# Kernel optimization log

Hardware: AMD Instinct MI355X
Metric: run time of the kernel (lower is better)

Reference implementation:

```python
import jax, jax.numpy as jnp
import numpy as np

N_NODES = 100000
N_EDGES = 3200000
NFEAT = 128
NHID = 128
NCLASS = 8
BN_EPS = 1e-5


def setup_inputs() -> dict:
    key = jax.random.key(0)
    ks = jax.random.split(key, 8)
    x = jax.random.normal(ks[0], (N_NODES, NFEAT), dtype=jnp.float32)
    edge_index = jax.random.randint(ks[1], (2, N_EDGES), 0, N_NODES, dtype=jnp.int64)
    # GCNConv params: weight [nfeat, nhid] (glorot), bias [nhid]
    lim = float(np.sqrt(6.0 / (NFEAT + NHID)))
    W = jax.random.uniform(ks[2], (NFEAT, NHID), minval=-lim, maxval=lim, dtype=jnp.float32)
    b_gc = jnp.zeros((NHID,), dtype=jnp.float32)
    # BatchNorm1d params
    gamma = jnp.ones((NHID,), dtype=jnp.float32)
    beta = jnp.zeros((NHID,), dtype=jnp.float32)
    # fc head: (nhid/2) -> nclass, xavier_uniform, zero bias
    lim2 = float(np.sqrt(6.0 / (NHID // 2 + NCLASS)))
    fc_w = jax.random.uniform(ks[3], (NCLASS, NHID // 2), minval=-lim2, maxval=lim2, dtype=jnp.float32)
    fc_b = jnp.zeros((NCLASS,), dtype=jnp.float32)
    return {"x": x, "edge_index": edge_index, "W": W, "b_gc": b_gc,
            "gamma": gamma, "beta": beta, "fc_w": fc_w, "fc_b": fc_b}


def _gcn_conv(x, edge_index, W, b):
    """PyG GCNConv: add self-loops, symmetric norm, linear, gather-scatter, bias."""
    N = x.shape[0]
    loops = jnp.arange(N, dtype=edge_index.dtype)
    src = jnp.concatenate([edge_index[0], loops])  # source (row / x_j)
    dst = jnp.concatenate([edge_index[1], loops])  # target (col / aggregation index)
    # degree of target nodes (edge weight = 1)
    deg = jax.ops.segment_sum(jnp.ones_like(dst, dtype=x.dtype), dst, num_segments=N)
    dinv = jnp.where(deg > 0, jax.lax.rsqrt(deg), 0.0)
    norm = dinv[src] * dinv[dst]  # [E+N]
    h = x @ W  # [N, nhid]
    msg = h[src] * norm[:, None]  # gather + scale
    out = jax.ops.segment_sum(msg, dst, num_segments=N)  # scatter-add
    return out + b


def _batchnorm(h, gamma, beta):
    mean = jnp.mean(h, axis=0)
    var = jnp.mean(jnp.square(h - mean), axis=0)  # biased, training-mode
    return gamma * (h - mean) * jax.lax.rsqrt(var + BN_EPS) + beta


def reference(x, edge_index, W, b_gc, gamma, beta, fc_w, fc_b):
    h = _gcn_conv(x, edge_index, W, b_gc)
    embed = _batchnorm(h, gamma, beta)
    half = embed.shape[1] // 2
    out = embed[:, :half] @ fc_w.T + fc_b
    return (out, embed)
```

## Files before the change

### kernel.cpp

```cpp
#include <hip/hip_runtime.h>
#include <hip/hip_bf16.h>
#include <math.h>

#define N_NODES 100000
#define N_EDGES 3200000
#define NFEAT 128
#define NHID 128
#define NCLASS 8
#define BN_EPS 1e-5f
#define CB 512
#define NBC 196
#define EPB 8192
#define PART_BLOCKS 391
#define GEMM_BLOCKS 1563

typedef __attribute__((ext_vector_type(8))) short short8;
typedef __attribute__((ext_vector_type(4))) float f32x4;

__device__ __forceinline__ short f2bf(float f) {
    __hip_bfloat16 b = __float2bfloat16(f);
    return *reinterpret_cast<short*>(&b);
}
__device__ __forceinline__ float bf_lo(unsigned u) { return __uint_as_float(u << 16); }
__device__ __forceinline__ float bf_hi(unsigned u) { return __uint_as_float(u & 0xffff0000u); }


#define WSTRIDE 136
#define XSTRIDE 136
__global__ __launch_bounds__(256) void k_prep(const float* __restrict__ x,
                                              const float* __restrict__ W,
                                              unsigned short* __restrict__ hb,
                                              const int* __restrict__ dst,
                                              int* __restrict__ ghist) {
    __shared__ __align__(16) short wlds[NHID * WSTRIDE];
    __shared__ __align__(16) short xl[64 * XSTRIDE];
    const int tid = threadIdx.x;

    if (blockIdx.x >= GEMM_BLOCKS) {
        __shared__ int lh[NBC];
        if (tid < NBC) lh[tid] = 0;
        __syncthreads();
        const int4* dst4 = (const int4*)dst;
        const int q0 = (blockIdx.x - GEMM_BLOCKS) * (EPB / 4) + tid;
#pragma unroll
        for (int i = 0; i < 8; ++i) {
            int q = q0 + i * 256;
            if (q < N_EDGES / 4) {
                int4 d = dst4[q];
                atomicAdd(&lh[d.x >> 9], 1);
                atomicAdd(&lh[d.y >> 9], 1);
                atomicAdd(&lh[d.z >> 9], 1);
                atomicAdd(&lh[d.w >> 9], 1);
            }
        }
        __syncthreads();
        if (tid < NBC) {
            int c = lh[tid];
            if (c) atomicAdd(&ghist[tid], c);
        }
        return;
    }

    const int row0 = blockIdx.x * 64;

#pragma unroll 8
    for (int i = 0; i < 64; ++i) {
        int idx = tid + i * 256;
        int k = idx >> 7, n = idx & 127;
        wlds[n * WSTRIDE + k] = f2bf(W[idx]);
    }
    const float4* x4 = (const float4*)x;
#pragma unroll
    for (int i = 0; i < 8; ++i) {
        int idx = tid + i * 256;
        int r = idx >> 5, c4 = idx & 31;
        int gr = row0 + r;
        float4 vv = (gr < N_NODES) ? x4[(size_t)gr * 32 + c4]
                                   : (float4){0.f, 0.f, 0.f, 0.f};
        short4 t;
        t.x = f2bf(vv.x); t.y = f2bf(vv.y); t.z = f2bf(vv.z); t.w = f2bf(vv.w);
        *(short4*)&xl[r * XSTRIDE + c4 * 4] = t;
    }
    __syncthreads();

    const int wid = tid >> 6, lane = tid & 63;
    const int qw = lane >> 4, lr = lane & 15;

    short8 a[4];
#pragma unroll
    for (int ks = 0; ks < 4; ++ks)
        a[ks] = *(const short8*)&xl[(wid * 16 + lr) * XSTRIDE + ks * 32 + qw * 8];

    f32x4 acc[8];
#pragma unroll
    for (int nt = 0; nt < 8; ++nt) acc[nt] = (f32x4){0.f, 0.f, 0.f, 0.f};

#pragma unroll
    for (int nt = 0; nt < 8; ++nt) {
#pragma unroll
        for (int ks = 0; ks < 4; ++ks) {
            short8 bfr = *(const short8*)&wlds[(nt * 16 + lr) * WSTRIDE + ks * 32 + qw * 8];
            acc[nt] = __builtin_amdgcn_mfma_f32_16x16x32_bf16(a[ks], bfr, acc[nt], 0, 0, 0);
        }
    }

    const int rbase = row0 + wid * 16 + qw * 4;
#pragma unroll
    for (int j = 0; j < 4; ++j) {
        int r = rbase + j;
        if (r >= N_NODES) continue;
#pragma unroll
        for (int nt = 0; nt < 8; ++nt)
            hb[(size_t)r * NHID + nt * 16 + lr] = (unsigned short)f2bf(acc[nt][j]);
    }
}


__global__ __launch_bounds__(512) void k_cscan(const int* __restrict__ ghist,
                                               int* __restrict__ coff,
                                               int* __restrict__ ccur,
                                               int* __restrict__ off,
                                               float* __restrict__ stats,
                                               int* __restrict__ ticket,
                                               unsigned short* __restrict__ hbzrow,
                                               float* __restrict__ dinv) {
    __shared__ int tmp[512];
    const int t = threadIdx.x;
    if (t < 256) stats[t] = 0.f;
    if (t == 0) { *ticket = 0; dinv[N_NODES] = 0.f; }
    if (t < NHID) hbzrow[t] = 0;
    int v = (t < NBC) ? ghist[t] : 0;
    tmp[t] = v;
    __syncthreads();
    for (int d = 1; d < 512; d <<= 1) {
        int u = (t >= d) ? tmp[t - d] : 0;
        __syncthreads();
        tmp[t] += u;
        __syncthreads();
    }
    int excl = tmp[t] - v;
    if (t < NBC) {
        coff[t] = excl;
        ccur[t] = excl;
    }
    if (t == NBC - 1) {
        coff[NBC] = tmp[t];
        off[N_NODES] = tmp[t];
    }
}


__global__ __launch_bounds__(256) void k_part(const int* __restrict__ src,
                                              const int* __restrict__ dst,
                                              int* __restrict__ ccur,
                                              unsigned* __restrict__ epack) {
    __shared__ int lh[NBC];
    __shared__ int lstart[NBC];
    __shared__ int adj[NBC];
    __shared__ int stmp[256];
    __shared__ unsigned sorted[EPB];
    __shared__ unsigned char bkt[EPB];
    const int tid = threadIdx.x;
    if (tid < NBC) lh[tid] = 0;
    __syncthreads();
    const int4* src4 = (const int4*)src;
    const int4* dst4 = (const int4*)dst;
    const int q0 = blockIdx.x * (EPB / 4) + tid;
    int4 sv[8], dv[8];
    int rk[32];
#pragma unroll
    for (int i = 0; i < 8; ++i) {
        int q = q0 + i * 256;
        if (q < N_EDGES / 4) {
            sv[i] = src4[q];
            dv[i] = dst4[q];
            rk[i * 4 + 0] = atomicAdd(&lh[dv[i].x >> 9], 1);
            rk[i * 4 + 1] = atomicAdd(&lh[dv[i].y >> 9], 1);
            rk[i * 4 + 2] = atomicAdd(&lh[dv[i].z >> 9], 1);
            rk[i * 4 + 3] = atomicAdd(&lh[dv[i].w >> 9], 1);
        } else dv[i].x = -1;
    }
    __syncthreads();
    int v = (tid < NBC) ? lh[tid] : 0;
    stmp[tid] = v;
    __syncthreads();
    for (int d = 1; d < 256; d <<= 1) {
        int u = (tid >= d) ? stmp[tid - d] : 0;
        __syncthreads();
        stmp[tid] += u;
        __syncthreads();
    }
    if (tid < NBC) {
        int ls = stmp[tid] - v;
        lstart[tid] = ls;
        adj[tid] = (v ? atomicAdd(&ccur[tid], v) : 0) - ls;
    }
    __syncthreads();
#pragma unroll
    for (int i = 0; i < 8; ++i) {
        if (dv[i].x >= 0) {
            int b, p;
            b = dv[i].x >> 9; p = lstart[b] + rk[i * 4 + 0];
            sorted[p] = ((unsigned)sv[i].x << 9) | (unsigned)(dv[i].x & 511); bkt[p] = (unsigned char)b;
            b = dv[i].y >> 9; p = lstart[b] + rk[i * 4 + 1];
            sorted[p] = ((unsigned)sv[i].y << 9) | (unsigned)(dv[i].y & 511); bkt[p] = (unsigned char)b;
            b = dv[i].z >> 9; p = lstart[b] + rk[i * 4 + 2];
            sorted[p] = ((unsigned)sv[i].z << 9) | (unsigned)(dv[i].z & 511); bkt[p] = (unsigned char)b;
            b = dv[i].w >> 9; p = lstart[b] + rk[i * 4 + 3];
            sorted[p] = ((unsigned)sv[i].w << 9) | (unsigned)(dv[i].w & 511); bkt[p] = (unsigned char)b;
        }
    }
    __syncthreads();
    const int vcnt = stmp[255];
    for (int p = tid; p < vcnt; p += 256)
        epack[p + adj[bkt[p]]] = sorted[p];
}


__global__ __launch_bounds__(256) void k_fine(const unsigned* __restrict__ epack,
                                              const int* __restrict__ coff,
                                              int* __restrict__ off,
                                              float* __restrict__ dinv,
                                              int* __restrict__ esrc) {
    __shared__ int lh[CB], lcur[CB], lsc[256];
    const int tid = threadIdx.x;
    const int b = blockIdx.x;
    const int node0 = b << 9;
    lh[tid] = 0;
    lh[tid + 256] = 0;
    __syncthreads();
    const int lo = coff[b], hiEnd = coff[b + 1];
    for (int i = lo + tid; i < hiEnd; i += 256)
        atomicAdd(&lh[epack[i] & 511u], 1);
    __syncthreads();
    int v0 = lh[2 * tid], v1 = lh[2 * tid + 1];
    int s = v0 + v1;
    lsc[tid] = s;
    __syncthreads();
    for (int d = 1; d < 256; d <<= 1) {
        int u = (tid >= d) ? lsc[tid - d] : 0;
        __syncthreads();
        lsc[tid] += u;
        __syncthreads();
    }
    int pairExcl = lsc[tid] - s;
    lcur[2 * tid] = pairExcl;
    lcur[2 * tid + 1] = pairExcl + v0;
    int n0 = node0 + 2 * tid, n1 = n0 + 1;
    if (n0 < N_NODES) { off[n0] = lo + pairExcl;      dinv[n0] = rsqrtf((float)(v0 + 1)); }
    if (n1 < N_NODES) { off[n1] = lo + pairExcl + v0; dinv[n1] = rsqrtf((float)(v1 + 1)); }
    __syncthreads();
    for (int i = lo + tid; i < hiEnd; i += 256) {
        unsigned p = epack[i];
        int pos = atomicAdd(&lcur[p & 511u], 1);
        esrc[lo + pos] = (int)(p >> 9);
    }
}


__global__ __launch_bounds__(256) void k_agg(const int* __restrict__ off,
                                             const int* __restrict__ esrc,
                                             const float* __restrict__ dinv,
                                             const uint2* __restrict__ hbq,
                                             float4* __restrict__ agg4) {
    const int node = (blockIdx.x << 2) | (threadIdx.x >> 6);
    const int lane = threadIdx.x & 63;
    const int hl = lane >> 5;
    const int cl = lane & 31;
    if (node >= N_NODES) return;

    const float dn = dinv[node];
    const int self = hl ? N_NODES : node;
    uint2 u0 = hbq[(size_t)self * 32 + cl];
    float aAx = dn * bf_lo(u0.x), aAy = dn * bf_hi(u0.x);
    float aAz = dn * bf_lo(u0.y), aAw = dn * bf_hi(u0.y);
    float aBx = 0.f, aBy = 0.f, aBz = 0.f, aBw = 0.f;
    float aCx = 0.f, aCy = 0.f, aCz = 0.f, aCw = 0.f;
    float aDx = 0.f, aDy = 0.f, aDz = 0.f, aDw = 0.f;

    const int begin = off[node], end = off[node + 1];
    for (int base = begin; base < end; base += 64) {
        int m = end - base;
        if (m > 64) m = 64;
        int sv = N_NODES;
        float dw = 0.f;
        if (lane < m) {
            sv = esrc[base + lane];
            dw = dinv[sv];
        }
        const int kmax = (m + 7) >> 3;
        for (int k = 0; k < kmax; ++k) {
            int sA = __shfl(sv, 8 * k + 0 + hl);
            int sB = __shfl(sv, 8 * k + 2 + hl);
            int sC = __shfl(sv, 8 * k + 4 + hl);
            int sD = __shfl(sv, 8 * k + 6 + hl);
            float wA = __shfl(dw, 8 * k + 0 + hl);
            float wB = __shfl(dw, 8 * k + 2 + hl);
            float wC = __shfl(dw, 8 * k + 4 + hl);
            float wD = __shfl(dw, 8 * k + 6 + hl);
            uint2 uA = hbq[(size_t)sA * 32 + cl];
            uint2 uB = hbq[(size_t)sB * 32 + cl];
            uint2 uC = hbq[(size_t)sC * 32 + cl];
            uint2 uD = hbq[(size_t)sD * 32 + cl];
            aAx = fmaf(wA, bf_lo(uA.x), aAx); aAy = fmaf(wA, bf_hi(uA.x), aAy);
            aAz = fmaf(wA, bf_lo(uA.y), aAz); aAw = fmaf(wA, bf_hi(uA.y), aAw);
            aBx = fmaf(wB, bf_lo(uB.x), aBx); aBy = fmaf(wB, bf_hi(uB.x), aBy);
            aBz = fmaf(wB, bf_lo(uB.y), aBz); aBw = fmaf(wB, bf_hi(uB.y), aBw);
            aCx = fmaf(wC, bf_lo(uC.x), aCx); aCy = fmaf(wC, bf_hi(uC.x), aCy);
            aCz = fmaf(wC, bf_lo(uC.y), aCz); aCw = fmaf(wC, bf_hi(uC.y), aCw);
            aDx = fmaf(wD, bf_lo(uD.x), aDx); aDy = fmaf(wD, bf_hi(uD.x), aDy);
            aDz = fmaf(wD, bf_lo(uD.y), aDz); aDw = fmaf(wD, bf_hi(uD.y), aDw);
        }
    }
    float ax = (aAx + aBx) + (aCx + aDx);
    float ay = (aAy + aBy) + (aCy + aDy);
    float az = (aAz + aBz) + (aCz + aDz);
    float aw = (aAw + aBw) + (aCw + aDw);
    ax += __shfl_xor(ax, 32);
    ay += __shfl_xor(ay, 32);
    az += __shfl_xor(az, 32);
    aw += __shfl_xor(aw, 32);
    if (hl == 0) {
        float4 o;
        o.x = ax * dn; o.y = ay * dn; o.z = az * dn; o.w = aw * dn;
        agg4[(size_t)node * 32 + cl] = o;
    }
}


__global__ __launch_bounds__(256) void k_stats(const float* __restrict__ agg,
                                               float* __restrict__ stats,
                                               int* __restrict__ ticket,
                                               const float* __restrict__ gamma,
                                               const float* __restrict__ beta,
                                               float* __restrict__ ss) {
    const int cb = threadIdx.x & 31;
    const int rg = threadIdx.x >> 5;
    const float4* a4 = (const float4*)agg;
    float4 s = {0.f, 0.f, 0.f, 0.f}, s2 = {0.f, 0.f, 0.f, 0.f};
    for (int r = blockIdx.x * 8 + rg; r < N_NODES; r += gridDim.x * 8) {
        float4 v = a4[(size_t)r * 32 + cb];
        s.x += v.x; s.y += v.y; s.z += v.z; s.w += v.w;
        s2.x += v.x * v.x; s2.y += v.y * v.y; s2.z += v.z * v.z; s2.w += v.w * v.w;
    }
    __shared__ float4 ls[256], ls2[256];
    __shared__ int lastflag;
    ls[threadIdx.x] = s;
    ls2[threadIdx.x] = s2;
    __syncthreads();
    if (rg == 0) {
        float4 ts = ls[cb], t2 = ls2[cb];
#pragma unroll
        for (int g = 1; g < 8; ++g) {
            float4 v = ls[g * 32 + cb], w = ls2[g * 32 + cb];
            ts.x += v.x; ts.y += v.y; ts.z += v.z; ts.w += v.w;
            t2.x += w.x; t2.y += w.y; t2.z += w.z; t2.w += w.w;
        }
        atomicAdd(&stats[cb * 4 + 0], ts.x);
        atomicAdd(&stats[cb * 4 + 1], ts.y);
        atomicAdd(&stats[cb * 4 + 2], ts.z);
        atomicAdd(&stats[cb * 4 + 3], ts.w);
        atomicAdd(&stats[128 + cb * 4 + 0], t2.x);
        atomicAdd(&stats[128 + cb * 4 + 1], t2.y);
        atomicAdd(&stats[128 + cb * 4 + 2], t2.z);
        atomicAdd(&stats[128 + cb * 4 + 3], t2.w);
    }
    __threadfence();
    __syncthreads();
    if (threadIdx.x == 0)
        lastflag = (atomicAdd(ticket, 1) == (int)gridDim.x - 1) ? 1 : 0;
    __syncthreads();
    if (lastflag && threadIdx.x < NHID) {
        int c = threadIdx.x;
        float sum = atomicAdd(&stats[c], 0.f);
        float sq  = atomicAdd(&stats[128 + c], 0.f);
        float mean = sum / (float)N_NODES;
        float var = fmaxf(sq / (float)N_NODES - mean * mean, 0.f);
        float inv = rsqrtf(var + BN_EPS);
        float sc = gamma[c] * inv;
        ss[c] = sc;
        ss[128 + c] = beta[c] - mean * sc;
    }
}


__global__ __launch_bounds__(256) void k_bnfc(float* __restrict__ embed,
                                              const float* __restrict__ ss,
                                              const float* __restrict__ fc_w,
                                              const float* __restrict__ fc_b,
                                              float* __restrict__ out) {
    __shared__ float se[64][68];
    __shared__ float sw[8][68];
    __shared__ float sb[8];
    const int tid = threadIdx.x;
    const int row0 = blockIdx.x * 64;
    {
        int d = tid;
        sw[d >> 6][d & 63] = fc_w[d];
        d = tid + 256;
        sw[d >> 6][d & 63] = fc_w[d];
        if (tid < 8) sb[tid] = fc_b[tid];
    }
    float4* ef4 = (float4*)embed;
    const float4* ssc4 = (const float4*)ss;
    const float4* ssh4 = (const float4*)(ss + 128);
#pragma unroll
    for (int i = 0; i < 8; ++i) {
        int d = tid + i * 256;
        int r = d >> 5;
        int cb = d & 31;
        int gr = row0 + r;
        if (gr < N_NODES) {
            float4 v = ef4[(size_t)gr * 32 + cb];
            float4 sc = ssc4[cb], sh = ssh4[cb];
            v.x = fmaf(v.x, sc.x, sh.x);
            v.y = fmaf(v.y, sc.y, sh.y);
            v.z = fmaf(v.z, sc.z, sh.z);
            v.w = fmaf(v.w, sc.w, sh.w);
            ef4[(size_t)gr * 32 + cb] = v;
            if (cb < 16) {
                se[r][cb * 4 + 0] = v.x; se[r][cb * 4 + 1] = v.y;
                se[r][cb * 4 + 2] = v.z; se[r][cb * 4 + 3] = v.w;
            }
        } else if (cb < 16) {
            se[r][cb * 4 + 0] = 0.f; se[r][cb * 4 + 1] = 0.f;
            se[r][cb * 4 + 2] = 0.f; se[r][cb * 4 + 3] = 0.f;
        }
    }
    __syncthreads();
    const int r = tid >> 2;
    const int j0 = (tid & 3) * 2;
    const int gr = row0 + r;
#pragma unroll
    for (int jj = 0; jj < 2; ++jj) {
        int j = j0 + jj;
        float s = sb[j];
#pragma unroll
        for (int k = 0; k < 64; ++k) s = fmaf(se[r][k], sw[j][k], s);
        if (gr < N_NODES) out[(size_t)gr * NCLASS + j] = s;
    }
}


extern "C" void kernel_launch(void* const* d_in, const int* in_sizes, int n_in,
                              void* d_out, int out_size, void* d_ws, size_t ws_size,
                              hipStream_t stream) {
    const float* x     = (const float*)d_in[0];
    const int*   ei    = (const int*)d_in[1];
    const float* W     = (const float*)d_in[2];
    const float* gamma = (const float*)d_in[4];
    const float* beta  = (const float*)d_in[5];
    const float* fc_w  = (const float*)d_in[6];
    const float* fc_b  = (const float*)d_in[7];

    const int* src = ei;
    const int* dst = ei + N_EDGES;

    float* out   = (float*)d_out;
    float* embed = (float*)d_out + (size_t)N_NODES * NCLASS;

    char* ws = (char*)d_ws;
    size_t o = 0;
    unsigned* epack = (unsigned*)(ws + o);          o += (size_t)N_EDGES * 4;
    unsigned short* hb = (unsigned short*)(ws + o); o += (size_t)(N_NODES + 1) * NHID * 2;
    o = (o + 255) & ~(size_t)255;
    int* esrc   = (int*)(ws + o);                   o += (size_t)N_EDGES * 4;
    int* off    = (int*)(ws + o);                   o += (size_t)(N_NODES + 1) * 4;
    float* dinv = (float*)(ws + o);                 o += (size_t)(N_NODES + 1) * 4;
    float* stats = (float*)(ws + o);                o += 256 * 4;
    float* ss    = (float*)(ws + o);                o += 256 * 4;
    int* ghist   = (int*)(ws + o);                  o += NBC * 4;
    int* coff    = (int*)(ws + o);                  o += (NBC + 1) * 4;
    int* ccur    = (int*)(ws + o);                  o += NBC * 4;
    int* ticket  = (int*)(ws + o);                  o += 4;

    hipMemsetAsync(ghist, 0, NBC * 4, stream);

    k_prep<<<GEMM_BLOCKS + PART_BLOCKS, 256, 0, stream>>>(x, W, hb, dst, ghist);

    k_cscan<<<1, 512, 0, stream>>>(ghist, coff, ccur, off, stats, ticket,
                                   hb + (size_t)N_NODES * NHID, dinv);
    k_part<<<PART_BLOCKS, 256, 0, stream>>>(src, dst, ccur, epack);
    k_fine<<<NBC, 256, 0, stream>>>(epack, coff, off, dinv, esrc);

    k_agg<<<(N_NODES + 3) / 4, 256, 0, stream>>>(off, esrc, dinv, (const uint2*)hb, (float4*)embed);

    k_stats<<<512, 256, 0, stream>>>(embed, stats, ticket, gamma, beta, ss);

    k_bnfc<<<(N_NODES + 63) / 64, 256, 0, stream>>>(embed, ss, fc_w, fc_b, out);
}
```

Baseline: 320.7 us.

## Prescale GEMM output by source dinv and fuse partition into GEMM launch

Per-node in-degrees are now counted with global atomics in a new count kernel, so dinv is ready before the GEMM. The GEMM epilogue multiplies each row by dinv[src], which lets the aggregation loop drop the per-edge dinv gather and its shuffles and use plain adds. The edge-partition pass is merged into the same launch as the GEMM so the two overlap. In exchange the count kernel adds 3.2M global atomics on per-node counters, and k_gp needs a larger shared-memory footprint.

```diff
diff --git a/kernel.cpp b/kernel.cpp
--- a/kernel.cpp
+++ b/kernel.cpp
@@ -25,49 +25,161 @@
 __device__ __forceinline__ float bf_hi(unsigned u) { return __uint_as_float(u & 0xffff0000u); }
 
 
-#define WSTRIDE 136
-#define XSTRIDE 136
-__global__ __launch_bounds__(256) void k_prep(const float* __restrict__ x,
-                                              const float* __restrict__ W,
-                                              unsigned short* __restrict__ hb,
-                                              const int* __restrict__ dst,
-                                              int* __restrict__ ghist) {
-    __shared__ __align__(16) short wlds[NHID * WSTRIDE];
-    __shared__ __align__(16) short xl[64 * XSTRIDE];
+__global__ __launch_bounds__(256) void k_cnt(const int* __restrict__ dst,
+                                             int* __restrict__ cnt,
+                                             int* __restrict__ ghist) {
+    __shared__ int lh[NBC];
     const int tid = threadIdx.x;
+    if (tid < NBC) lh[tid] = 0;
+    __syncthreads();
+    const int4* dst4 = (const int4*)dst;
+    const int q0 = blockIdx.x * (EPB / 4) + tid;
+#pragma unroll
+    for (int i = 0; i < 8; ++i) {
+        int q = q0 + i * 256;
+        if (q < N_EDGES / 4) {
+            int4 d = dst4[q];
+            atomicAdd(&cnt[d.x], 1);
+            atomicAdd(&cnt[d.y], 1);
+            atomicAdd(&cnt[d.z], 1);
+            atomicAdd(&cnt[d.w], 1);
+            atomicAdd(&lh[d.x >> 9], 1);
+            atomicAdd(&lh[d.y >> 9], 1);
+            atomicAdd(&lh[d.z >> 9], 1);
+            atomicAdd(&lh[d.w >> 9], 1);
+        }
+    }
+    __syncthreads();
+    if (tid < NBC) {
+        int c = lh[tid];
+        if (c) atomicAdd(&ghist[tid], c);
+    }
+}
+
+
+__global__ __launch_bounds__(512) void k_scan(const int* __restrict__ ghist,
+                                              const int* __restrict__ cnt,
+                                              int* __restrict__ coff,
+                                              int* __restrict__ ccur,
+                                              int* __restrict__ off,
+                                              float* __restrict__ dinv,
+                                              float* __restrict__ stats,
+                                              int* __restrict__ ticket,
+                                              unsigned short* __restrict__ hbzrow) {
+    const int t = threadIdx.x;
+    if (blockIdx.x > 0) {
+        int node = (blockIdx.x - 1) * 512 + t;
+        if (node < N_NODES) dinv[node] = rsqrtf((float)(cnt[node] + 1));
+        return;
+    }
+    __shared__ int tmp[512];
+    if (t < 256) stats[t] = 0.f;
+    if (t == 0) *ticket = 0;
+    if (t < NHID) hbzrow[t] = 0;
+    int v = (t < NBC) ? ghist[t] : 0;
+    tmp[t] = v;
+    __syncthreads();
+    for (int d = 1; d < 512; d <<= 1) {
+        int u = (t >= d) ? tmp[t - d] : 0;
+        __syncthreads();
+        tmp[t] += u;
+        __syncthreads();
+    }
+    int excl = tmp[t] - v;
+    if (t < NBC) {
+        coff[t] = excl;
+        ccur[t] = excl;
+    }
+    if (t == NBC - 1) {
+        coff[NBC] = tmp[t];
+        off[N_NODES] = tmp[t];
+    }
+}
+
+
+__global__ __launch_bounds__(256) void k_gp(const float* __restrict__ x,
+                                            const float* __restrict__ W,
+                                            const float* __restrict__ dinv,
+                                            unsigned short* __restrict__ hb,
+                                            const int* __restrict__ src,
+                                            const int* __restrict__ dst,
+                                            int* __restrict__ ccur,
+                                            unsigned* __restrict__ epack) {
+    __shared__ __align__(16) char smem[52224];
+    const int tid = threadIdx.x;
 
     if (blockIdx.x >= GEMM_BLOCKS) {
-        __shared__ int lh[NBC];
+        unsigned* sorted = (unsigned*)smem;
+        unsigned char* bkt = (unsigned char*)(smem + 32768);
+        int* lh     = (int*)(smem + 40960);
+        int* lstart = (int*)(smem + 40960 + 784);
+        int* adj    = (int*)(smem + 40960 + 1568);
+        int* stmp   = (int*)(smem + 40960 + 2352);
         if (tid < NBC) lh[tid] = 0;
         __syncthreads();
+        const int4* src4 = (const int4*)src;
         const int4* dst4 = (const int4*)dst;
         const int q0 = (blockIdx.x - GEMM_BLOCKS) * (EPB / 4) + tid;
+        int4 sv[8], dv[8];
+        int rk[32];
 #pragma unroll
         for (int i = 0; i < 8; ++i) {
             int q = q0 + i * 256;
             if (q < N_EDGES / 4) {
-                int4 d = dst4[q];
-                atomicAdd(&lh[d.x >> 9], 1);
-                atomicAdd(&lh[d.y >> 9], 1);
-                atomicAdd(&lh[d.z >> 9], 1);
-                atomicAdd(&lh[d.w >> 9], 1);
+                sv[i] = src4[q];
+                dv[i] = dst4[q];
+                rk[i * 4 + 0] = atomicAdd(&lh[dv[i].x >> 9], 1);
+                rk[i * 4 + 1] = atomicAdd(&lh[dv[i].y >> 9], 1);
+                rk[i * 4 + 2] = atomicAdd(&lh[dv[i].z >> 9], 1);
+                rk[i * 4 + 3] = atomicAdd(&lh[dv[i].w >> 9], 1);
+            } else dv[i].x = -1;
+        }
+        __syncthreads();
+        int v = (tid < NBC) ? lh[tid] : 0;
+        stmp[tid] = v;
+        __syncthreads();
+        for (int d = 1; d < 256; d <<= 1) {
+            int u = (tid >= d) ? stmp[tid - d] : 0;
+            __syncthreads();
+            stmp[tid] += u;
+            __syncthreads();
+        }
+        if (tid < NBC) {
+            int ls = stmp[tid] - v;
+            lstart[tid] = ls;
+            adj[tid] = (v ? atomicAdd(&ccur[tid], v) : 0) - ls;
+        }
+        __syncthreads();
+#pragma unroll
+        for (int i = 0; i < 8; ++i) {
+            if (dv[i].x >= 0) {
+                int b, p;
+                b = dv[i].x >> 9; p = lstart[b] + rk[i * 4 + 0];
+                sorted[p] = ((unsigned)sv[i].x << 9) | (unsigned)(dv[i].x & 511); bkt[p] = (unsigned char)b;
+                b = dv[i].y >> 9; p = lstart[b] + rk[i * 4 + 1];
+                sorted[p] = ((unsigned)sv[i].y << 9) | (unsigned)(dv[i].y & 511); bkt[p] = (unsigned char)b;
+                b = dv[i].z >> 9; p = lstart[b] + rk[i * 4 + 2];
+                sorted[p] = ((unsigned)sv[i].z << 9) | (unsigned)(dv[i].z & 511); bkt[p] = (unsigned char)b;
+                b = dv[i].w >> 9; p = lstart[b] + rk[i * 4 + 3];
+                sorted[p] = ((unsigned)sv[i].w << 9) | (unsigned)(dv[i].w & 511); bkt[p] = (unsigned char)b;
             }
         }
         __syncthreads();
-        if (tid < NBC) {
-            int c = lh[tid];
-            if (c) atomicAdd(&ghist[tid], c);
-        }
+        const int vcnt = stmp[255];
+        for (int p = tid; p < vcnt; p += 256)
+            epack[p + adj[bkt[p]]] = sorted[p];
         return;
     }
 
+    short* wlds = (short*)smem;
+    short* xl   = (short*)(smem + 34816);
     const int row0 = blockIdx.x * 64;
 
 #pragma unroll 8
     for (int i = 0; i < 64; ++i) {
         int idx = tid + i * 256;
         int k = idx >> 7, n = idx & 127;
-        wlds[n * WSTRIDE + k] = f2bf(W[idx]);
+        wlds[n * 136 + k] = f2bf(W[idx]);
     }
     const float4* x4 = (const float4*)x;
 #pragma unroll
@@ -79,7 +191,7 @@
                                    : (float4){0.f, 0.f, 0.f, 0.f};
         short4 t;
         t.x = f2bf(vv.x); t.y = f2bf(vv.y); t.z = f2bf(vv.z); t.w = f2bf(vv.w);
-        *(short4*)&xl[r * XSTRIDE + c4 * 4] = t;
+        *(short4*)&xl[r * 136 + c4 * 4] = t;
     }
     __syncthreads();
 
@@ -89,7 +201,7 @@
     short8 a[4];
 #pragma unroll
     for (int ks = 0; ks < 4; ++ks)
-        a[ks] = *(const short8*)&xl[(wid * 16 + lr) * XSTRIDE + ks * 32 + qw * 8];
+        a[ks] = *(const short8*)&xl[(wid * 16 + lr) * 136 + ks * 32 + qw * 8];
 
     f32x4 acc[8];
 #pragma unroll
@@ -99,128 +211,29 @@
     for (int nt = 0; nt < 8; ++nt) {
 #pragma unroll
         for (int ks = 0; ks < 4; ++ks) {
-            short8 bfr = *(const short8*)&wlds[(nt * 16 + lr) * WSTRIDE + ks * 32 + qw * 8];
+            short8 bfr = *(const short8*)&wlds[(nt * 16 + lr) * 136 + ks * 32 + qw * 8];
             acc[nt] = __builtin_amdgcn_mfma_f32_16x16x32_bf16(a[ks], bfr, acc[nt], 0, 0, 0);
         }
     }
 
     const int rbase = row0 + wid * 16 + qw * 4;
+    float dvv[4];
+#pragma unroll
+    for (int j = 0; j < 4; ++j) dvv[j] = (rbase + j < N_NODES) ? dinv[rbase + j] : 0.f;
 #pragma unroll
     for (int j = 0; j < 4; ++j) {
         int r = rbase + j;
         if (r >= N_NODES) continue;
 #pragma unroll
         for (int nt = 0; nt < 8; ++nt)
-            hb[(size_t)r * NHID + nt * 16 + lr] = (unsigned short)f2bf(acc[nt][j]);
-    }
-}
-
-
-__global__ __launch_bounds__(512) void k_cscan(const int* __restrict__ ghist,
-                                               int* __restrict__ coff,
-                                               int* __restrict__ ccur,
-                                               int* __restrict__ off,
-                                               float* __restrict__ stats,
-                                               int* __restrict__ ticket,
-                                               unsigned short* __restrict__ hbzrow,
-                                               float* __restrict__ dinv) {
-    __shared__ int tmp[512];
-    const int t = threadIdx.x;
-    if (t < 256) stats[t] = 0.f;
-    if (t == 0) { *ticket = 0; dinv[N_NODES] = 0.f; }
-    if (t < NHID) hbzrow[t] = 0;
-    int v = (t < NBC) ? ghist[t] : 0;
-    tmp[t] = v;
-    __syncthreads();
-    for (int d = 1; d < 512; d <<= 1) {
-        int u = (t >= d) ? tmp[t - d] : 0;
-        __syncthreads();
-        tmp[t] += u;
-        __syncthreads();
-    }
-    int excl = tmp[t] - v;
-    if (t < NBC) {
-        coff[t] = excl;
-        ccur[t] = excl;
-    }
-    if (t == NBC - 1) {
-        coff[NBC] = tmp[t];
-        off[N_NODES] = tmp[t];
-    }
-}
-
-
-__global__ __launch_bounds__(256) void k_part(const int* __restrict__ src,
-                                              const int* __restrict__ dst,
-                                              int* __restrict__ ccur,
-                                              unsigned* __restrict__ epack) {
-    __shared__ int lh[NBC];
-    __shared__ int lstart[NBC];
-    __shared__ int adj[NBC];
-    __shared__ int stmp[256];
-    __shared__ unsigned sorted[EPB];
-    __shared__ unsigned char bkt[EPB];
-    const int tid = threadIdx.x;
-    if (tid < NBC) lh[tid] = 0;
-    __syncthreads();
-    const int4* src4 = (const int4*)src;
-    const int4* dst4 = (const int4*)dst;
-    const int q0 = blockIdx.x * (EPB / 4) + tid;
-    int4 sv[8], dv[8];
-    int rk[32];
-#pragma unroll
-    for (int i = 0; i < 8; ++i) {
-        int q = q0 + i * 256;
-        if (q < N_EDGES / 4) {
-            sv[i] = src4[q];
-            dv[i] = dst4[q];
-            rk[i * 4 + 0] = atomicAdd(&lh[dv[i].x >> 9], 1);
-            rk[i * 4 + 1] = atomicAdd(&lh[dv[i].y >> 9], 1);
-            rk[i * 4 + 2] = atomicAdd(&lh[dv[i].z >> 9], 1);
-            rk[i * 4 + 3] = atomicAdd(&lh[dv[i].w >> 9], 1);
-        } else dv[i].x = -1;
-    }
-    __syncthreads();
-    int v = (tid < NBC) ? lh[tid] : 0;
-    stmp[tid] = v;
-    __syncthreads();
-    for (int d = 1; d < 256; d <<= 1) {
-        int u = (tid >= d) ? stmp[tid - d] : 0;
-        __syncthreads();
-        stmp[tid] += u;
-        __syncthreads();
-    }
-    if (tid < NBC) {
-        int ls = stmp[tid] - v;
-        lstart[tid] = ls;
-        adj[tid] = (v ? atomicAdd(&ccur[tid], v) : 0) - ls;
-    }
-    __syncthreads();
-#pragma unroll
-    for (int i = 0; i < 8; ++i) {
-        if (dv[i].x >= 0) {
-            int b, p;
-            b = dv[i].x >> 9; p = lstart[b] + rk[i * 4 + 0];
-            sorted[p] = ((unsigned)sv[i].x << 9) | (unsigned)(dv[i].x & 511); bkt[p] = (unsigned char)b;
-            b = dv[i].y >> 9; p = lstart[b] + rk[i * 4 + 1];
-            sorted[p] = ((unsigned)sv[i].y << 9) | (unsigned)(dv[i].y & 511); bkt[p] = (unsigned char)b;
-            b = dv[i].z >> 9; p = lstart[b] + rk[i * 4 + 2];
-            sorted[p] = ((unsigned)sv[i].z << 9) | (unsigned)(dv[i].z & 511); bkt[p] = (unsigned char)b;
-            b = dv[i].w >> 9; p = lstart[b] + rk[i * 4 + 3];
-            sorted[p] = ((unsigned)sv[i].w << 9) | (unsigned)(dv[i].w & 511); bkt[p] = (unsigned char)b;
-        }
-    }
-    __syncthreads();
-    const int vcnt = stmp[255];
-    for (int p = tid; p < vcnt; p += 256)
-        epack[p + adj[bkt[p]]] = sorted[p];
+            hb[(size_t)r * NHID + nt * 16 + lr] = (unsigned short)f2bf(dvv[j] * acc[nt][j]);
+    }
 }
 
 
 __global__ __launch_bounds__(256) void k_fine(const unsigned* __restrict__ epack,
                                               const int* __restrict__ coff,
                                               int* __restrict__ off,
-                                              float* __restrict__ dinv,
                                               int* __restrict__ esrc) {
     __shared__ int lh[CB], lcur[CB], lsc[256];
     const int tid = threadIdx.x;
@@ -247,8 +260,8 @@
     lcur[2 * tid] = pairExcl;
     lcur[2 * tid + 1] = pairExcl + v0;
     int n0 = node0 + 2 * tid, n1 = n0 + 1;
-    if (n0 < N_NODES) { off[n0] = lo + pairExcl;      dinv[n0] = rsqrtf((float)(v0 + 1)); }
-    if (n1 < N_NODES) { off[n1] = lo + pairExcl + v0; dinv[n1] = rsqrtf((float)(v1 + 1)); }
+    if (n0 < N_NODES) off[n0] = lo + pairExcl;
+    if (n1 < N_NODES) off[n1] = lo + pairExcl + v0;
     __syncthreads();
     for (int i = lo + tid; i < hiEnd; i += 256) {
         unsigned p = epack[i];
@@ -272,8 +285,7 @@
     const float dn = dinv[node];
     const int self = hl ? N_NODES : node;
     uint2 u0 = hbq[(size_t)self * 32 + cl];
-    float aAx = dn * bf_lo(u0.x), aAy = dn * bf_hi(u0.x);
-    float aAz = dn * bf_lo(u0.y), aAw = dn * bf_hi(u0.y);
+    float aAx = bf_lo(u0.x), aAy = bf_hi(u0.x), aAz = bf_lo(u0.y), aAw = bf_hi(u0.y);
     float aBx = 0.f, aBy = 0.f, aBz = 0.f, aBw = 0.f;
     float aCx = 0.f, aCy = 0.f, aCz = 0.f, aCw = 0.f;
     float aDx = 0.f, aDy = 0.f, aDz = 0.f, aDw = 0.f;
@@ -282,34 +294,21 @@
     for (int base = begin; base < end; base += 64) {
         int m = end - base;
         if (m > 64) m = 64;
-        int sv = N_NODES;
-        float dw = 0.f;
-        if (lane < m) {
-            sv = esrc[base + lane];
-            dw = dinv[sv];
-        }
+        int sv = (lane < m) ? esrc[base + lane] : N_NODES;
         const int kmax = (m + 7) >> 3;
         for (int k = 0; k < kmax; ++k) {
             int sA = __shfl(sv, 8 * k + 0 + hl);
             int sB = __shfl(sv, 8 * k + 2 + hl);
             int sC = __shfl(sv, 8 * k + 4 + hl);
             int sD = __shfl(sv, 8 * k + 6 + hl);
-            float wA = __shfl(dw, 8 * k + 0 + hl);
-            float wB = __shfl(dw, 8 * k + 2 + hl);
-            float wC = __shfl(dw, 8 * k + 4 + hl);
-            float wD = __shfl(dw, 8 * k + 6 + hl);
             uint2 uA = hbq[(size_t)sA * 32 + cl];
             uint2 uB = hbq[(size_t)sB * 32 + cl];
             uint2 uC = hbq[(size_t)sC * 32 + cl];
             uint2 uD = hbq[(size_t)sD * 32 + cl];
-            aAx = fmaf(wA, bf_lo(uA.x), aAx); aAy = fmaf(wA, bf_hi(uA.x), aAy);
-            aAz = fmaf(wA, bf_lo(uA.y), aAz); aAw = fmaf(wA, bf_hi(uA.y), aAw);
-            aBx = fmaf(wB, bf_lo(uB.x), aBx); aBy = fmaf(wB, bf_hi(uB.x), aBy);
-            aBz = fmaf(wB, bf_lo(uB.y), aBz); aBw = fmaf(wB, bf_hi(uB.y), aBw);
-            aCx = fmaf(wC, bf_lo(uC.x), aCx); aCy = fmaf(wC, bf_hi(uC.x), aCy);
-            aCz = fmaf(wC, bf_lo(uC.y), aCz); aCw = fmaf(wC, bf_hi(uC.y), aCw);
-            aDx = fmaf(wD, bf_lo(uD.x), aDx); aDy = fmaf(wD, bf_hi(uD.x), aDy);
-            aDz = fmaf(wD, bf_lo(uD.y), aDz); aDw = fmaf(wD, bf_hi(uD.y), aDw);
+            aAx += bf_lo(uA.x); aAy += bf_hi(uA.x); aAz += bf_lo(uA.y); aAw += bf_hi(uA.y);
+            aBx += bf_lo(uB.x); aBy += bf_hi(uB.x); aBz += bf_lo(uB.y); aBw += bf_hi(uB.y);
+            aCx += bf_lo(uC.x); aCy += bf_hi(uC.x); aCz += bf_lo(uC.y); aCw += bf_hi(uC.y);
+            aDx += bf_lo(uD.x); aDy += bf_hi(uD.x); aDz += bf_lo(uD.y); aDw += bf_hi(uD.y);
         }
     }
     float ax = (aAx + aBx) + (aCx + aDx);
@@ -466,22 +465,26 @@
     o = (o + 255) & ~(size_t)255;
     int* esrc   = (int*)(ws + o);                   o += (size_t)N_EDGES * 4;
     int* off    = (int*)(ws + o);                   o += (size_t)(N_NODES + 1) * 4;
-    float* dinv = (float*)(ws + o);                 o += (size_t)(N_NODES + 1) * 4;
+    float* dinv = (float*)(ws + o);                 o += (size_t)N_NODES * 4;
+    int* cnt    = (int*)(ws + o);                   o += (size_t)N_NODES * 4;
+    int* ghist  = (int*)(ws + o);                   o += NBC * 4;
     float* stats = (float*)(ws + o);                o += 256 * 4;
     float* ss    = (float*)(ws + o);                o += 256 * 4;
-    int* ghist   = (int*)(ws + o);                  o += NBC * 4;
     int* coff    = (int*)(ws + o);                  o += (NBC + 1) * 4;
     int* ccur    = (int*)(ws + o);                  o += NBC * 4;
     int* ticket  = (int*)(ws + o);                  o += 4;
 
-    hipMemsetAsync(ghist, 0, NBC * 4, stream);
-
-    k_prep<<<GEMM_BLOCKS + PART_BLOCKS, 256, 0, stream>>>(x, W, hb, dst, ghist);
-
-    k_cscan<<<1, 512, 0, stream>>>(ghist, coff, ccur, off, stats, ticket,
-                                   hb + (size_t)N_NODES * NHID, dinv);
-    k_part<<<PART_BLOCKS, 256, 0, stream>>>(src, dst, ccur, epack);
-    k_fine<<<NBC, 256, 0, stream>>>(epack, coff, off, dinv, esrc);
+    hipMemsetAsync(cnt, 0, (size_t)(N_NODES + NBC) * 4, stream);
+
+    k_cnt<<<PART_BLOCKS, 256, 0, stream>>>(dst, cnt, ghist);
+
+    k_scan<<<1 + NBC, 512, 0, stream>>>(ghist, cnt, coff, ccur, off, dinv,
+                                        stats, ticket, hb + (size_t)N_NODES * NHID);
+
+    k_gp<<<GEMM_BLOCKS + PART_BLOCKS, 256, 0, stream>>>(x, W, dinv, hb,
+                                                        src, dst, ccur, epack);
+
+    k_fine<<<NBC, 256, 0, stream>>>(epack, coff, off, esrc);
 
     k_agg<<<(N_NODES + 3) / 4, 256, 0, stream>>>(off, esrc, dinv, (const uint2*)hb, (float4*)embed);
 
```

After: 444.9 us. 1.39x slower.
